# Kernel optimization log

Measured on AMD Instinct MI355X. Metric: run time of the kernel, lower is better.

The kernel has to match this reference:

```python
import jax, jax.numpy as jnp
import numpy as np
from jax import lax

BOX_STRIDES = (32, 64, 128, 256)
MASK_STRIDE = 4
MASK_SIZE = 28
PATCH = 512
TOPK = 64
SCORE_TH = 0.5
IOU_TH = 0.5
MASK_TH = 0.5


def setup_inputs():
    key = jax.random.key(0)
    ks = jax.random.split(key, 10)
    d = {}
    d["pred0"] = jax.random.normal(ks[0], (2, 6, 16, 16), jnp.float32)
    d["pred1"] = jax.random.normal(ks[1], (2, 6, 8, 8), jnp.float32)
    d["pred2"] = jax.random.normal(ks[2], (2, 6, 4, 4), jnp.float32)
    d["pred3"] = jax.random.normal(ks[3], (2, 6, 2, 2), jnp.float32)
    d["feat0"] = jax.random.normal(ks[4], (2, 64, 128, 128), jnp.float32)
    d["feat1"] = jax.random.normal(ks[5], (2, 64, 64, 64), jnp.float32)
    d["feat2"] = jax.random.normal(ks[6], (2, 64, 32, 32), jnp.float32)
    d["feat3"] = jax.random.normal(ks[7], (2, 64, 16, 16), jnp.float32)
    d["w1"] = jax.random.normal(ks[8], (128, 256, 3, 3), jnp.float32) * 0.05
    d["b1"] = jnp.zeros((128,), jnp.float32)
    d["w2"] = jax.random.normal(ks[9], (1, 128, 1, 1), jnp.float32) * 0.05
    d["b2"] = jnp.zeros((1,), jnp.float32)
    return d


def _decode_level(pred, stride):
    # pred: [B, 6, H, W] -> [B, H*W, 6], (cx,cy)=(p+grid)*stride, wh=exp(p)*stride
    B, no, H, W = pred.shape
    p = pred.transpose(0, 2, 3, 1).reshape(B, H * W, no)
    gy, gx = jnp.meshgrid(jnp.arange(H), jnp.arange(W), indexing="ij")
    grid = jnp.stack([gx.ravel(), gy.ravel()], axis=-1).astype(p.dtype)  # [HW,2] (x,y)
    xy = (p[..., 0:2] + grid) * stride
    wh = jnp.exp(p[..., 2:4]) * stride
    return jnp.concatenate([xy, wh, p[..., 4:]], axis=-1)


def _iou_matrix(b):
    # b: [K,4] xyxy
    area = jnp.clip(b[:, 2] - b[:, 0], 0) * jnp.clip(b[:, 3] - b[:, 1], 0)
    ix0 = jnp.maximum(b[:, None, 0], b[None, :, 0])
    iy0 = jnp.maximum(b[:, None, 1], b[None, :, 1])
    ix1 = jnp.minimum(b[:, None, 2], b[None, :, 2])
    iy1 = jnp.minimum(b[:, None, 3], b[None, :, 3])
    inter = jnp.clip(ix1 - ix0, 0) * jnp.clip(iy1 - iy0, 0)
    union = area[:, None] + area[None, :] - inter
    return inter / jnp.maximum(union, 1e-9)


def _nms_keep(boxes, labels, valid):
    # boxes already sorted by descending score; batched NMS via per-class coord offset
    off = labels.astype(boxes.dtype)[:, None] * (PATCH * 8.0)
    iou = _iou_matrix(boxes + off)
    idx = jnp.arange(TOPK)

    def body(i, keep):
        sup = keep[i] & (iou[i] > IOU_TH) & (idx > i)
        return keep & ~sup

    return lax.fori_loop(0, TOPK, body, valid)


def _roi_align_one(feat, box):
    # feat: [C,Hf,Wf]; box: [4] xyxy in image coords (spatial_scale=1/MASK_STRIDE)
    # torchvision-style aligned=False, one bilinear sample per bin center
    C, Hf, Wf = feat.shape
    b = box / MASK_STRIDE
    bw = (b[2] - b[0]) / MASK_SIZE
    bh = (b[3] - b[1]) / MASK_SIZE
    xs = b[0] + (jnp.arange(MASK_SIZE, dtype=feat.dtype) + 0.5) * bw
    ys = b[1] + (jnp.arange(MASK_SIZE, dtype=feat.dtype) + 0.5) * bh
    x = jnp.clip(jnp.broadcast_to(xs[None, :], (MASK_SIZE, MASK_SIZE)), 0.0, Wf - 1.0)
    y = jnp.clip(jnp.broadcast_to(ys[:, None], (MASK_SIZE, MASK_SIZE)), 0.0, Hf - 1.0)
    x0 = jnp.floor(x).astype(jnp.int32)
    y0 = jnp.floor(y).astype(jnp.int32)
    x1 = jnp.minimum(x0 + 1, Wf - 1)
    y1 = jnp.minimum(y0 + 1, Hf - 1)
    fx = x - x0
    fy = y - y0
    v00 = feat[:, y0, x0]
    v01 = feat[:, y0, x1]
    v10 = feat[:, y1, x0]
    v11 = feat[:, y1, x1]
    return (v00 * (1 - fy) * (1 - fx) + v01 * (1 - fy) * fx
            + v10 * fy * (1 - fx) + v11 * fy * fx)  # [C,S,S]


def _paste_one(mask_soft, box_int):
    # nearest-neighbor upsample of [S,S] mask into its box on a [P,P] canvas
    x0, y0, x1, y1 = box_int[0], box_int[1], box_int[2], box_int[3]
    h = y1 - y0 + 1
    w = x1 - x0 + 1
    ys = jnp.arange(PATCH, dtype=jnp.int32)
    xs = jnp.arange(PATCH, dtype=jnp.int32)
    iy = jnp.clip((ys - y0) * MASK_SIZE // h, 0, MASK_SIZE - 1)
    ix = jnp.clip((xs - x0) * MASK_SIZE // w, 0, MASK_SIZE - 1)
    g = mask_soft[iy][:, ix]  # [P,P]
    inside = ((ys >= y0) & (ys <= y1))[:, None] & ((xs >= x0) & (xs <= x1))[None, :]
    return jnp.where(inside, g, 0.0)


def _conv(x, w, b, pad):
    y = lax.conv_general_dilated(x, w, (1, 1), pad, dimension_numbers=("NCHW", "OIHW", "NCHW"))
    return y + b[None, :, None, None]


def _pipeline(pred0, pred1, pred2, pred3, feat0, feat1, feat2, feat3, w1, b1, w2, b2):
    # box branch: decode per-level predictions
    yolo = jnp.concatenate(
        [_decode_level(p, s) for p, s in zip([pred0, pred1, pred2, pred3], BOX_STRIDES)],
        axis=1,
    )  # [B,N,6]
    B = yolo.shape[0]
    cx, cy, w_, h_ = yolo[..., 0], yolo[..., 1], yolo[..., 2], yolo[..., 3]
    boxes = jnp.stack([cx - w_ / 2, cy - h_ / 2, cx + w_ / 2, cy + h_ / 2], axis=-1)
    scores = jax.nn.sigmoid(yolo[..., 4])
    labels = jnp.argmax(yolo[..., 5:], axis=-1)
    valid = scores > SCORE_TH
    top_scores, top_idx = lax.top_k(jnp.where(valid, scores, 0.0), TOPK)
    boxes_k = jnp.take_along_axis(boxes, top_idx[..., None], axis=1)  # [B,K,4]
    labels_k = jnp.take_along_axis(labels, top_idx, axis=1)
    valid_k = top_scores > SCORE_TH
    keep = jax.vmap(_nms_keep)(boxes_k, labels_k, valid_k)  # [B,K] bool

    # mask branch: merge mask feats at the first level's resolution (nearest)
    H0, W0 = feat0.shape[2], feat0.shape[3]
    merged = jnp.concatenate(
        [feat0] + [jax.image.resize(f, (B, f.shape[1], H0, W0), "nearest") for f in [feat1, feat2, feat3]],
        axis=1,
    )  # [B,256,H0,W0]
    rois = jax.vmap(lambda f, bx: jax.vmap(lambda bb: _roi_align_one(f, bb))(bx))(merged, boxes_k)
    C = rois.shape[2]
    x = rois.reshape(B * TOPK, C, MASK_SIZE, MASK_SIZE)
    hdn = jax.nn.silu(_conv(x, w1, b1, "SAME"))
    logits = _conv(hdn, w2, b2, "SAME")  # [B*K,1,S,S]
    soft = jax.nn.sigmoid(logits).reshape(B, TOPK, MASK_SIZE, MASK_SIZE)

    box_int = jnp.clip(boxes_k, 0, PATCH - 1).astype(jnp.int32)
    pasted = jax.vmap(jax.vmap(_paste_one))(soft, box_int)  # [B,K,P,P]
    return top_scores, boxes_k, labels_k, pasted, keep


def reference(pred0, pred1, pred2, pred3, feat0, feat1, feat2, feat3, w1, b1, w2, b2):
    top_scores, boxes_k, labels_k, pasted, keep = _pipeline(
        pred0, pred1, pred2, pred3, feat0, feat1, feat2, feat3, w1, b1, w2, b2
    )
    out_scores = top_scores * keep
    bin_masks = (pasted > MASK_TH) & keep[:, :, None, None]
    return out_scores, boxes_k, labels_k.astype(jnp.int32), bin_masks, keep
```

## Files before the change

### kernel.cpp

```cpp
#include <hip/hip_runtime.h>
#include <hip/hip_bf16.h>
#include <cstdint>

#define NTOPK 64
#define A_TOT 340
#define MS 28

#define OFF_SCORES 0
#define OFF_BOXES  128
#define OFF_LABELS 640
#define OFF_MASKS  768
#define OFF_KEEP   33555200ull

typedef __attribute__((ext_vector_type(4))) float f32x4;
typedef long fp8x8;

__device__ __forceinline__ float sigmoidf_(float x) { return 1.f / (1.f + expf(-x)); }
__device__ __forceinline__ float bf2f(unsigned u) {
  return __uint_as_float(u << 16);
}
__device__ __forceinline__ unsigned short f2bf(float f) {
  __hip_bfloat16 h = __float2bfloat16(f);
  return *(unsigned short*)&h;
}

__global__ __launch_bounds__(256) void k_prep(
    const float* __restrict__ p0, const float* __restrict__ p1,
    const float* __restrict__ p2, const float* __restrict__ p3,
    const float* __restrict__ f0, const float* __restrict__ f1,
    const float* __restrict__ f2, const float* __restrict__ f3,
    const float* __restrict__ w1,
    float* __restrict__ out,
    float* __restrict__ ws_boxes, int* __restrict__ ws_keep,
    int* __restrict__ ws_boxint,
    unsigned char* __restrict__ wt, unsigned short* __restrict__ mg)
{
  __shared__ __align__(16) char smem_raw[128 * 260 * 2];
  const int bid = blockIdx.x;
  const int t = threadIdx.x;

  if (bid < 2) {
    const int b = bid;
    float* sc = (float*)smem_raw;
    float(*bx)[4] = (float(*)[4])(sc + A_TOT);
    float* tk_score = (float*)(bx + A_TOT);
    float(*tk_box)[4] = (float(*)[4])(tk_score + 64);

    for (int a = t; a < A_TOT; a += 256) {
      const float* pp; int W, HW, la; float stride;
      if (a < 256)      { pp = p0; W = 16; HW = 256; la = a;       stride = 32.f;  }
      else if (a < 320) { pp = p1; W = 8;  HW = 64;  la = a - 256; stride = 64.f;  }
      else if (a < 336) { pp = p2; W = 4;  HW = 16;  la = a - 320; stride = 128.f; }
      else              { pp = p3; W = 2;  HW = 4;   la = a - 336; stride = 256.f; }
      const float* base = pp + (size_t)b * 6 * HW + la;
      float v0 = base[0], v1 = base[HW], v2 = base[2 * HW], v3 = base[3 * HW], v4 = base[4 * HW];
      int gx = la % W, gy = la / W;
      float cx = (v0 + (float)gx) * stride;
      float cy = (v1 + (float)gy) * stride;
      float w_ = expf(v2) * stride;
      float h_ = expf(v3) * stride;
      float score = sigmoidf_(v4);
      sc[a] = (score > 0.5f) ? score : 0.f;
      bx[a][0] = cx - 0.5f * w_;
      bx[a][1] = cy - 0.5f * h_;
      bx[a][2] = cx + 0.5f * w_;
      bx[a][3] = cy + 0.5f * h_;
    }
    __syncthreads();

    for (int a = t; a < A_TOT; a += 256) {
      float my = sc[a];
      int rank = 0;
      for (int j = 0; j < A_TOT; ++j) {
        float o = sc[j];
        rank += (o > my) || (o == my && j < a);
      }
      if (rank < NTOPK) {
        tk_score[rank] = my;
        tk_box[rank][0] = bx[a][0];
        tk_box[rank][1] = bx[a][1];
        tk_box[rank][2] = bx[a][2];
        tk_box[rank][3] = bx[a][3];
      }
    }
    __syncthreads();

    if (t < NTOPK) {
      float x0 = tk_box[t][0], y0 = tk_box[t][1];
      float x1 = tk_box[t][2], y1 = tk_box[t][3];
      float s = tk_score[t];
      float area = fmaxf(x1 - x0, 0.f) * fmaxf(y1 - y0, 0.f);
      int keep = (s > 0.5f) ? 1 : 0;
      for (int i = 0; i < NTOPK - 1; ++i) {
        int   ki = __shfl(keep, i);
        float a0 = __shfl(x0, i);
        float c0 = __shfl(y0, i);
        float a1 = __shfl(x1, i);
        float c1 = __shfl(y1, i);
        float ai = __shfl(area, i);
        if (ki && t > i && keep) {
          float ix0 = fmaxf(a0, x0), iy0 = fmaxf(c0, y0);
          float ix1 = fminf(a1, x1), iy1 = fminf(c1, y1);
          float inter = fmaxf(ix1 - ix0, 0.f) * fmaxf(iy1 - iy0, 0.f);
          float uni = ai + area - inter;
          float iou = inter / fmaxf(uni, 1e-9f);
          if (iou > 0.5f) keep = 0;
        }
      }
      int box = b * NTOPK + t;
      out[OFF_SCORES + box] = keep ? s : 0.f;
      float bv[4] = {x0, y0, x1, y1};
      #pragma unroll
      for (int c = 0; c < 4; ++c) {
        out[OFF_BOXES + box * 4 + c] = bv[c];
        ws_boxes[box * 4 + c] = bv[c];
        float bc = fminf(fmaxf(bv[c], 0.f), 511.f);
        ws_boxint[box * 4 + c] = (int)bc;
      }
      out[OFF_LABELS + box] = 0.f;
      out[OFF_KEEP + box] = keep ? 1.f : 0.f;
      ws_keep[box] = keep;
    }
    return;
  }

  if (bid < 130) {
    const int co = bid - 2;
    const int ci = t;
    const int c = ci >> 5, cil = ci & 31;
    const int cq = co >> 5, col = co & 31;
    const int slot = ((cil >> 3) ^ ((col >> 2) & 3)) * 8 + (cil & 7);
    const float* src = w1 + ((size_t)co * 256 + ci) * 9;
    #pragma unroll
    for (int tap = 0; tap < 9; ++tap) {
      unsigned u = __builtin_amdgcn_cvt_pk_fp8_f32(src[tap], 0.f, 0, false);
      wt[(((size_t)(cq * 8 + c) * 9 + tap)) * 1024 + col * 32 + slot] =
          (unsigned char)(u & 0xff);
    }
    return;
  }

  {
    const int idx = bid - 130;
    const int b = idx >> 7;
    const int y = idx & 127;
    unsigned short* tile = (unsigned short*)smem_raw;
    const int x = t & 127, ch = t >> 7;

    {
      const float* src = f0 + ((size_t)b * 64) * 16384 + y * 128 + x;
      for (int cc = 0; cc < 32; ++cc) {
        int cl = ch * 32 + cc;
        tile[x * 260 + cl] = f2bf(src[(size_t)cl * 16384]);
      }
    }
    {
      const float* src = f1 + ((size_t)b * 64) * 4096 + (y >> 1) * 64 + (x >> 1);
      for (int cc = 0; cc < 32; ++cc) {
        int cl = ch * 32 + cc;
        tile[x * 260 + 64 + cl] = f2bf(src[(size_t)cl * 4096]);
      }
    }
    {
      const float* src = f2 + ((size_t)b * 64) * 1024 + (y >> 2) * 32 + (x >> 2);
      for (int cc = 0; cc < 32; ++cc) {
        int cl = ch * 32 + cc;
        tile[x * 260 + 128 + cl] = f2bf(src[(size_t)cl * 1024]);
      }
    }
    {
      const float* src = f3 + ((size_t)b * 64) * 256 + (y >> 3) * 16 + (x >> 3);
      for (int cc = 0; cc < 32; ++cc) {
        int cl = ch * 32 + cc;
        tile[x * 260 + 192 + cl] = f2bf(src[(size_t)cl * 256]);
      }
    }
    __syncthreads();
    unsigned short* dst = mg + (((size_t)b * 128 + y) * 128) * 256;
    for (int it = 0; it < 32; ++it) {
      int qq = t + it * 256;
      int xx = qq >> 6, cg = qq & 63;
      *(ushort4*)(dst + xx * 256 + cg * 4) = *(ushort4*)&tile[xx * 260 + cg * 4];
    }
  }
}

__global__ __launch_bounds__(256) void k_roistage(
    const unsigned short* __restrict__ mg,
    const float* __restrict__ ws_boxes, const int* __restrict__ ws_keep,
    unsigned char* __restrict__ roi)
{
  const int boxLo = blockIdx.x & 7;
  const int r2 = blockIdx.x >> 3;
  const int r = r2 % 30;
  const int box = ((r2 / 30) << 3) | boxLo;
  if (!ws_keep[box]) return;
  const int t = threadIdx.x;
  unsigned char* rbox = roi + (size_t)box * 8 * 30 * 1024;
  const int gr = r - 1;

  if (gr < 0 || gr > 27) {
    uint2 z = {0u, 0u};
    for (int e = t; e < 1024; e += 256) {
      int chunk = e >> 7, rem = e & 127;
      int cell = rem >> 2, quad = rem & 3;
      size_t off = ((size_t)(chunk * 30 + r)) * 1024 + cell * 32 +
                   (quad ^ ((cell >> 2) & 3)) * 8;
      *(uint2*)(rbox + off) = z;
    }
    return;
  }

  __shared__ int   xa_s[MS], xb_s[MS];
  __shared__ float fx_s[MS];
  __shared__ float by_s[4];
  if (t < 4) by_s[t] = ws_boxes[box * 4 + t];
  __syncthreads();
  const float b0 = by_s[0] * 0.25f, b1_ = by_s[1] * 0.25f;
  const float b2_ = by_s[2] * 0.25f, b3_ = by_s[3] * 0.25f;
  if (t < MS) {
    float bw = (b2_ - b0) * (1.f / MS);
    float x = b0 + ((float)t + 0.5f) * bw;
    x = fminf(fmaxf(x, 0.f), 127.f);
    int x0 = (int)floorf(x);
    xa_s[t] = x0; xb_s[t] = min(x0 + 1, 127); fx_s[t] = x - (float)x0;
  }
  float bh = (b3_ - b1_) * (1.f / MS);
  float yy = b1_ + ((float)gr + 0.5f) * bh;
  yy = fminf(fmaxf(yy, 0.f), 127.f);
  int ya = (int)floorf(yy);
  int yb = min(ya + 1, 127);
  float fy = yy - (float)ya;
  __syncthreads();

  const int b = box >> 6;
  const unsigned short* mgb = mg + ((size_t)b * 128 * 128) * 256;

  for (int e = t; e < 1024; e += 256) {
    int chunk = e >> 7, rem = e & 127;
    int cell = rem >> 2, quad = rem & 3;
    size_t off = ((size_t)(chunk * 30 + r)) * 1024 + cell * 32 +
                 (quad ^ ((cell >> 2) & 3)) * 8;
    int gc = cell - 1;
    if (gc < 0 || gc > 27) {
      uint2 z = {0u, 0u};
      *(uint2*)(rbox + off) = z;
      continue;
    }
    int U = chunk * 4 + quad;
    int xa = xa_s[gc], xb = xb_s[gc];
    float fx = fx_s[gc];
    float w00 = (1.f - fy) * (1.f - fx), w01 = (1.f - fy) * fx;
    float w10 = fy * (1.f - fx),         w11 = fy * fx;
    uint4 A = *(const uint4*)(mgb + ((size_t)(ya * 128 + xa)) * 256 + U * 8);
    uint4 B = *(const uint4*)(mgb + ((size_t)(ya * 128 + xb)) * 256 + U * 8);
    uint4 C = *(const uint4*)(mgb + ((size_t)(yb * 128 + xa)) * 256 + U * 8);
    uint4 D = *(const uint4*)(mgb + ((size_t)(yb * 128 + xb)) * 256 + U * 8);
    const unsigned* pa = (const unsigned*)&A;
    const unsigned* pb = (const unsigned*)&B;
    const unsigned* pc = (const unsigned*)&C;
    const unsigned* pd = (const unsigned*)&D;
    float f[8];
    #pragma unroll
    for (int k2 = 0; k2 < 4; ++k2) {
      f[2 * k2] = bf2f(pa[k2] & 0xffffu) * w00 + bf2f(pb[k2] & 0xffffu) * w01 +
                  bf2f(pc[k2] & 0xffffu) * w10 + bf2f(pd[k2] & 0xffffu) * w11;
      f[2 * k2 + 1] = bf2f(pa[k2] >> 16) * w00 + bf2f(pb[k2] >> 16) * w01 +
                      bf2f(pc[k2] >> 16) * w10 + bf2f(pd[k2] >> 16) * w11;
    }
    unsigned o0 = __builtin_amdgcn_cvt_pk_fp8_f32(f[0], f[1], 0, false);
    o0 = __builtin_amdgcn_cvt_pk_fp8_f32(f[2], f[3], o0, true);
    unsigned o1 = __builtin_amdgcn_cvt_pk_fp8_f32(f[4], f[5], 0, false);
    o1 = __builtin_amdgcn_cvt_pk_fp8_f32(f[6], f[7], o1, true);
    uint2 pk; pk.x = o0; pk.y = o1;
    *(uint2*)(rbox + off) = pk;
  }
}

__global__ __launch_bounds__(256, 4) void k_conv(
    const unsigned char* __restrict__ roi,
    const unsigned char* __restrict__ wt,
    const float* __restrict__ b1, const float* __restrict__ w2,
    const int* __restrict__ ws_keep,
    float* __restrict__ ws_logit4)
{
  const int bid = blockIdx.x;
  const int boxLo = bid & 7;
  const int r1 = bid >> 3;
  const int cq = r1 & 3;
  const int q = (r1 >> 2) & 3;
  const int box = ((r1 >> 4) << 3) | boxLo;
  if (!ws_keep[box]) return;
  const int t = threadIdx.x;
  const int lane = t & 63, wv = t >> 6;
  const int laneN = lane & 15, kg = lane >> 4;

  __shared__ __align__(16) unsigned char lds[18432];

  int badd[4][3];
  bool act[4];
  #pragma unroll
  for (int i = 0; i < 4; ++i) {
    int tile = wv * 4 + i;
    act[i] = (tile * 16) < 196;
    int p = tile * 16 + laneN;
    if (p > 195) p = 195;
    int py = p / 28, px = p - py * 28;
    #pragma unroll
    for (int dx = 0; dx < 3; ++dx) {
      int cell = px + dx;
      badd[i][dx] = 9216 + py * 1024 + cell * 32 + (kg ^ ((cell >> 2) & 3)) * 8;
    }
  }
  const int aswz = (kg ^ ((laneN >> 2) & 3)) * 8;

  f32x4 acc[2][4];
  #pragma unroll
  for (int m = 0; m < 2; ++m)
    #pragma unroll
    for (int i = 0; i < 4; ++i) acc[m][i] = (f32x4){0.f, 0.f, 0.f, 0.f};

  const uint4* rbase = (const uint4*)roi;
  const uint4* wbase = (const uint4*)wt;

  uint4 ga0, ga1, ga2;
  uint4 gb0, gb1, gb2;
  auto issue_load = [&](int c) {
    const uint4* wa = wbase + (size_t)(cq * 8 + c) * 576;
    ga0 = wa[t]; ga1 = wa[t + 256];
    if (t < 64) ga2 = wa[t + 512];
    const uint4* s = rbase + ((size_t)(box * 8 + c) * 30 + q * 7) * 64;
    gb0 = s[t]; gb1 = s[t + 256];
    if (t < 64) gb2 = s[t + 512];
  };

  issue_load(0);
  #pragma unroll 1
  for (int c = 0; c < 8; ++c) {
    {
      uint4* da = (uint4*)lds;
      da[t] = ga0; da[t + 256] = ga1;
      if (t < 64) da[t + 512] = ga2;
      uint4* db = (uint4*)(lds + 9216);
      db[t] = gb0; db[t + 256] = gb1;
      if (t < 64) db[t + 512] = gb2;
    }
    __syncthreads();
    if (c < 7) issue_load(c + 1);
    #pragma unroll
    for (int tap = 0; tap < 9; ++tap) {
      const int dy = tap / 3, dx = tap % 3;
      fp8x8 av0 = *(const fp8x8*)(lds + tap * 1024 + laneN * 32 + aswz);
      fp8x8 av1 = *(const fp8x8*)(lds + tap * 1024 + 512 + laneN * 32 + aswz);
      #pragma unroll
      for (int i = 0; i < 4; ++i) {
        if (act[i]) {
          fp8x8 bv = *(const fp8x8*)(lds + badd[i][dx] + dy * 1024);
          acc[0][i] = __builtin_amdgcn_mfma_f32_16x16x32_fp8_fp8(av0, bv, acc[0][i], 0, 0, 0);
          acc[1][i] = __builtin_amdgcn_mfma_f32_16x16x32_fp8_fp8(av1, bv, acc[1][i], 0, 0, 0);
        }
      }
    }
    __syncthreads();
  }

  float b1v[2][4], w2v[2][4];
  #pragma unroll
  for (int m = 0; m < 2; ++m)
    #pragma unroll
    for (int r = 0; r < 4; ++r) {
      int co = cq * 32 + m * 16 + kg * 4 + r;
      b1v[m][r] = b1[co];
      w2v[m][r] = w2[co];
    }
  #pragma unroll
  for (int i = 0; i < 4; ++i) {
    if (!act[i]) continue;
    float part = 0.f;
    #pragma unroll
    for (int m = 0; m < 2; ++m)
      #pragma unroll
      for (int r = 0; r < 4; ++r) {
        float h = acc[m][i][r] + b1v[m][r];
        part = fmaf(w2v[m][r], h * sigmoidf_(h), part);
      }
    part += __shfl_xor(part, 16);
    part += __shfl_xor(part, 32);
    int p = (wv * 4 + i) * 16 + laneN;
    if (kg == 0 && p < 196)
      ws_logit4[((size_t)box * 4 + cq) * 784 + q * 196 + p] = part;
  }
}

__global__ __launch_bounds__(256) void k_paste(
    const float* __restrict__ ws_logit4, const int* __restrict__ ws_keep,
    const int* __restrict__ ws_boxint, const float* __restrict__ b2,
    float* __restrict__ out)
{
  const int box = blockIdx.x >> 4;
  const int yo  = blockIdx.x & 15;
  const int t = threadIdx.x;
  float* mb = out + OFF_MASKS + (size_t)box * 262144 + (size_t)yo * 32 * 512;

  if (!ws_keep[box]) {
    f32x4 z = {0.f, 0.f, 0.f, 0.f};
    f32x4* p = (f32x4*)mb;
    for (int e = t; e < 4096; e += 256)
      __builtin_nontemporal_store(z, p + e);
    return;
  }

  __shared__ float soft[784];
  __shared__ int iys[32];
  __shared__ int bi[4];
  if (t < 4) bi[t] = ws_boxint[box * 4 + t];
  __syncthreads();
  const int x0 = bi[0], y0 = bi[1], x1 = bi[2], y1 = bi[3];
  const int w = x1 - x0 + 1, h = y1 - y0 + 1;
  const float b2v = b2[0];
  const float* l0 = ws_logit4 + (size_t)box * 4 * 784;

  for (int e = t; e < 784; e += 256)
    soft[e] = sigmoidf_(l0[e] + l0[784 + e] + l0[1568 + e] + l0[2352 + e] + b2v);
  if (t < 32) {
    int Y = yo * 32 + t;
    int vy = (Y - y0) * MS;
    int iy = (vy >= 0) ? (vy / h) : 0;
    iys[t] = min(max(iy, 0), MS - 1);
  }
  __syncthreads();

  const int c4 = (t & 127) * 4;
  const int rr = t >> 7;
  int ixr[4];
  bool inx[4];
  #pragma unroll
  for (int u = 0; u < 4; ++u) {
    int X = c4 + u;
    int vx = (X - x0) * MS;
    int ix = (vx >= 0) ? (vx / w) : 0;
    ixr[u] = min(max(ix, 0), MS - 1);
    inx[u] = (X >= x0) && (X <= x1);
  }

  int prev_iy = -1;
  f32x4 v = {0.f, 0.f, 0.f, 0.f};
  #pragma unroll 1
  for (int it = 0; it < 16; ++it) {
    int Yl = it * 2 + rr;
    int Y = yo * 32 + Yl;
    f32x4 o;
    if (Y >= y0 && Y <= y1) {
      int iy = iys[Yl];
      if (iy != prev_iy) {
        prev_iy = iy;
        #pragma unroll
        for (int u = 0; u < 4; ++u)
          v[u] = (inx[u] && soft[iy * MS + ixr[u]] > 0.5f) ? 1.f : 0.f;
      }
      o = v;
    } else {
      o = (f32x4){0.f, 0.f, 0.f, 0.f};
    }
    __builtin_nontemporal_store(o, (f32x4*)(mb + (size_t)Yl * 512 + c4));
  }
}

extern "C" void kernel_launch(void* const* d_in, const int* in_sizes, int n_in,
                              void* d_out, int out_size, void* d_ws, size_t ws_size,
                              hipStream_t stream) {
  const float* p0 = (const float*)d_in[0];
  const float* p1 = (const float*)d_in[1];
  const float* p2 = (const float*)d_in[2];
  const float* p3 = (const float*)d_in[3];
  const float* f0 = (const float*)d_in[4];
  const float* f1 = (const float*)d_in[5];
  const float* f2 = (const float*)d_in[6];
  const float* f3 = (const float*)d_in[7];
  const float* w1 = (const float*)d_in[8];
  const float* b1 = (const float*)d_in[9];
  const float* w2 = (const float*)d_in[10];
  const float* b2 = (const float*)d_in[11];
  float* out = (float*)d_out;

  float* wsf = (float*)d_ws;
  float*          ws_boxes  = wsf;
  int*            ws_keep   = (int*)(wsf + 512);
  int*            ws_boxint = (int*)(wsf + 640);
  float*          ws_logit4 = wsf + 1152;
  unsigned char*  ws_wt     = (unsigned char*)(wsf + 402560);
  unsigned short* ws_merged = (unsigned short*)(wsf + 476288);
  unsigned char*  ws_roi    = (unsigned char*)(wsf + 4670592);

  k_prep<<<386, 256, 0, stream>>>(p0, p1, p2, p3, f0, f1, f2, f3, w1,
                                  out, ws_boxes, ws_keep, ws_boxint,
                                  ws_wt, ws_merged);
  k_roistage<<<3840, 256, 0, stream>>>(ws_merged, ws_boxes, ws_keep, ws_roi);
  k_conv<<<2048, 256, 0, stream>>>(ws_roi, ws_wt, b1, w2, ws_keep, ws_logit4);
  k_paste<<<2048, 256, 0, stream>>>(ws_logit4, ws_keep, ws_boxint, b2, out);
}
```

Before: 263.8 us.

## Double-buffer ROI tiles in LDS, read weights from global, rotate tile assignment

The conv kernel now double-buffers the ROI input tile in LDS, so only one barrier per channel chunk is needed instead of two, and it stops staging weights in LDS, reading the fp8 weight fragments directly from global/cache memory instead. Tile-to-wave assignment is interleaved (tile = rot + 4*i) with a per-block rotation, which balances the inactive tail tiles across waves. This aims to cut barrier stalls and LDS store traffic. The cost is per-tap global-memory latency on the A-operand loads.

```diff
diff --git a/kernel.cpp b/kernel.cpp
--- a/kernel.cpp
+++ b/kernel.cpp
@@ -295,13 +295,15 @@
   const int lane = t & 63, wv = t >> 6;
   const int laneN = lane & 15, kg = lane >> 4;
 
-  __shared__ __align__(16) unsigned char lds[18432];
+  const int rot = (wv + (bid >> 3)) & 3;
+
+  __shared__ __align__(16) unsigned char lds[2][9216];
 
   int badd[4][3];
   bool act[4];
   #pragma unroll
   for (int i = 0; i < 4; ++i) {
-    int tile = wv * 4 + i;
+    int tile = rot + 4 * i;
     act[i] = (tile * 16) < 196;
     int p = tile * 16 + laneN;
     if (p > 195) p = 195;
@@ -309,7 +311,7 @@
     #pragma unroll
     for (int dx = 0; dx < 3; ++dx) {
       int cell = px + dx;
-      badd[i][dx] = 9216 + py * 1024 + cell * 32 + (kg ^ ((cell >> 2) & 3)) * 8;
+      badd[i][dx] = py * 1024 + cell * 32 + (kg ^ ((cell >> 2) & 3)) * 8;
     }
   }
   const int aswz = (kg ^ ((laneN >> 2) & 3)) * 8;
@@ -321,47 +323,49 @@
     for (int i = 0; i < 4; ++i) acc[m][i] = (f32x4){0.f, 0.f, 0.f, 0.f};
 
   const uint4* rbase = (const uint4*)roi;
-  const uint4* wbase = (const uint4*)wt;
-
-  uint4 ga0, ga1, ga2;
+  const unsigned char* wbase = wt + (size_t)cq * 8 * 9216;
+
   uint4 gb0, gb1, gb2;
   auto issue_load = [&](int c) {
-    const uint4* wa = wbase + (size_t)(cq * 8 + c) * 576;
-    ga0 = wa[t]; ga1 = wa[t + 256];
-    if (t < 64) ga2 = wa[t + 512];
     const uint4* s = rbase + ((size_t)(box * 8 + c) * 30 + q * 7) * 64;
     gb0 = s[t]; gb1 = s[t + 256];
     if (t < 64) gb2 = s[t + 512];
   };
+  auto write_lds = [&](int buf) {
+    uint4* db = (uint4*)lds[buf];
+    db[t] = gb0; db[t + 256] = gb1;
+    if (t < 64) db[t + 512] = gb2;
+  };
 
   issue_load(0);
+  write_lds(0);
+  __syncthreads();
+
+  int cur = 0;
   #pragma unroll 1
   for (int c = 0; c < 8; ++c) {
-    {
-      uint4* da = (uint4*)lds;
-      da[t] = ga0; da[t + 256] = ga1;
-      if (t < 64) da[t + 512] = ga2;
-      uint4* db = (uint4*)(lds + 9216);
-      db[t] = gb0; db[t + 256] = gb1;
-      if (t < 64) db[t + 512] = gb2;
-    }
-    __syncthreads();
     if (c < 7) issue_load(c + 1);
+    const unsigned char* wa = wbase + (size_t)c * 9216;
+    const unsigned char* bb = lds[cur];
     #pragma unroll
     for (int tap = 0; tap < 9; ++tap) {
       const int dy = tap / 3, dx = tap % 3;
-      fp8x8 av0 = *(const fp8x8*)(lds + tap * 1024 + laneN * 32 + aswz);
-      fp8x8 av1 = *(const fp8x8*)(lds + tap * 1024 + 512 + laneN * 32 + aswz);
+      fp8x8 av0 = *(const fp8x8*)(wa + tap * 1024 + laneN * 32 + aswz);
+      fp8x8 av1 = *(const fp8x8*)(wa + tap * 1024 + 512 + laneN * 32 + aswz);
       #pragma unroll
       for (int i = 0; i < 4; ++i) {
         if (act[i]) {
-          fp8x8 bv = *(const fp8x8*)(lds + badd[i][dx] + dy * 1024);
+          fp8x8 bv = *(const fp8x8*)(bb + badd[i][dx] + dy * 1024);
           acc[0][i] = __builtin_amdgcn_mfma_f32_16x16x32_fp8_fp8(av0, bv, acc[0][i], 0, 0, 0);
           acc[1][i] = __builtin_amdgcn_mfma_f32_16x16x32_fp8_fp8(av1, bv, acc[1][i], 0, 0, 0);
         }
       }
     }
-    __syncthreads();
+    if (c < 7) {
+      write_lds(cur ^ 1);
+      __syncthreads();
+      cur ^= 1;
+    }
   }
 
   float b1v[2][4], w2v[2][4];
@@ -386,7 +390,7 @@
       }
     part += __shfl_xor(part, 16);
     part += __shfl_xor(part, 32);
-    int p = (wv * 4 + i) * 16 + laneN;
+    int p = (rot + 4 * i) * 16 + laneN;
     if (kg == 0 && p < 196)
       ws_logit4[((size_t)box * 4 + cq) * 784 + q * 196 + p] = part;
   }
```

After: 271.4 us. 1.03x slower.

## Merge output-channel quarters into one conv block to share ROI tile loads

Applied to the files above, without the earlier changes.

The weight tensor layout is reordered so all four output-channel quarters for an input chunk are contiguous. The conv kernel now runs 512-thread blocks where each pair of waves owns one channel quarter, so one ROI tile load in LDS is shared by all 128 output channels instead of being reloaded by four separate blocks. This cuts redundant ROI global traffic and block count. In exchange it uses more LDS (about 45 KB), more accumulator registers per wave (7 tiles), and fewer, larger blocks, which may lower occupancy.

```diff
diff --git a/kernel.cpp b/kernel.cpp
--- a/kernel.cpp
+++ b/kernel.cpp
@@ -134,7 +134,7 @@
     #pragma unroll
     for (int tap = 0; tap < 9; ++tap) {
       unsigned u = __builtin_amdgcn_cvt_pk_fp8_f32(src[tap], 0.f, 0, false);
-      wt[(((size_t)(cq * 8 + c) * 9 + tap)) * 1024 + col * 32 + slot] =
+      wt[(((size_t)(c * 4 + cq) * 9 + tap)) * 1024 + col * 32 + slot] =
           (unsigned char)(u & 0xff);
     }
     return;
@@ -277,7 +277,7 @@
   }
 }
 
-__global__ __launch_bounds__(256, 4) void k_conv(
+__global__ __launch_bounds__(512, 4) void k_conv(
     const unsigned char* __restrict__ roi,
     const unsigned char* __restrict__ wt,
     const float* __restrict__ b1, const float* __restrict__ w2,
@@ -287,73 +287,76 @@
   const int bid = blockIdx.x;
   const int boxLo = bid & 7;
   const int r1 = bid >> 3;
-  const int cq = r1 & 3;
-  const int q = (r1 >> 2) & 3;
-  const int box = ((r1 >> 4) << 3) | boxLo;
+  const int q = r1 & 3;
+  const int box = ((r1 >> 2) << 3) | boxLo;
   if (!ws_keep[box]) return;
   const int t = threadIdx.x;
   const int lane = t & 63, wv = t >> 6;
+  const int cq = wv >> 1, half = wv & 1;
   const int laneN = lane & 15, kg = lane >> 4;
 
-  __shared__ __align__(16) unsigned char lds[18432];
-
-  int badd[4][3];
-  bool act[4];
+  __shared__ __align__(16) unsigned char lds[46080];
+
+  int badd[7][3];
+  bool act[7];
   #pragma unroll
-  for (int i = 0; i < 4; ++i) {
-    int tile = wv * 4 + i;
-    act[i] = (tile * 16) < 196;
+  for (int i = 0; i < 7; ++i) {
+    int tile = half * 7 + i;
+    act[i] = tile < 13;
     int p = tile * 16 + laneN;
     if (p > 195) p = 195;
     int py = p / 28, px = p - py * 28;
     #pragma unroll
     for (int dx = 0; dx < 3; ++dx) {
       int cell = px + dx;
-      badd[i][dx] = 9216 + py * 1024 + cell * 32 + (kg ^ ((cell >> 2) & 3)) * 8;
+      badd[i][dx] = 36864 + py * 1024 + cell * 32 + (kg ^ ((cell >> 2) & 3)) * 8;
     }
   }
   const int aswz = (kg ^ ((laneN >> 2) & 3)) * 8;
 
-  f32x4 acc[2][4];
+  f32x4 acc[2][7];
   #pragma unroll
   for (int m = 0; m < 2; ++m)
     #pragma unroll
-    for (int i = 0; i < 4; ++i) acc[m][i] = (f32x4){0.f, 0.f, 0.f, 0.f};
+    for (int i = 0; i < 7; ++i) acc[m][i] = (f32x4){0.f, 0.f, 0.f, 0.f};
 
   const uint4* rbase = (const uint4*)roi;
   const uint4* wbase = (const uint4*)wt;
 
-  uint4 ga0, ga1, ga2;
-  uint4 gb0, gb1, gb2;
+  uint4 ga0, ga1, ga2, ga3, ga4;
+  uint4 gb0, gb1;
   auto issue_load = [&](int c) {
-    const uint4* wa = wbase + (size_t)(cq * 8 + c) * 576;
-    ga0 = wa[t]; ga1 = wa[t + 256];
-    if (t < 64) ga2 = wa[t + 512];
+    const uint4* wa = wbase + (size_t)c * 2304;
+    ga0 = wa[t]; ga1 = wa[t + 512]; ga2 = wa[t + 1024]; ga3 = wa[t + 1536];
+    if (t < 256) ga4 = wa[t + 2048];
     const uint4* s = rbase + ((size_t)(box * 8 + c) * 30 + q * 7) * 64;
-    gb0 = s[t]; gb1 = s[t + 256];
-    if (t < 64) gb2 = s[t + 512];
+    gb0 = s[t];
+    if (t < 64) gb1 = s[t + 512];
   };
+  auto write_lds = [&]() {
+    uint4* da = (uint4*)lds;
+    da[t] = ga0; da[t + 512] = ga1; da[t + 1024] = ga2; da[t + 1536] = ga3;
+    if (t < 256) da[t + 2048] = ga4;
+    uint4* db = (uint4*)(lds + 36864);
+    db[t] = gb0;
+    if (t < 64) db[t + 512] = gb1;
+  };
 
   issue_load(0);
+  const unsigned char* la = lds + (size_t)cq * 9216;
+
   #pragma unroll 1
   for (int c = 0; c < 8; ++c) {
-    {
-      uint4* da = (uint4*)lds;
-      da[t] = ga0; da[t + 256] = ga1;
-      if (t < 64) da[t + 512] = ga2;
-      uint4* db = (uint4*)(lds + 9216);
-      db[t] = gb0; db[t + 256] = gb1;
-      if (t < 64) db[t + 512] = gb2;
-    }
+    write_lds();
     __syncthreads();
     if (c < 7) issue_load(c + 1);
     #pragma unroll
     for (int tap = 0; tap < 9; ++tap) {
-      const int dy = tap / 3, dx = tap % 3;
-      fp8x8 av0 = *(const fp8x8*)(lds + tap * 1024 + laneN * 32 + aswz);
-      fp8x8 av1 = *(const fp8x8*)(lds + tap * 1024 + 512 + laneN * 32 + aswz);
+      const int dy = tap / 3, dx = tap - dy * 3;
+      fp8x8 av0 = *(const fp8x8*)(la + tap * 1024 + laneN * 32 + aswz);
+      fp8x8 av1 = *(const fp8x8*)(la + tap * 1024 + 512 + laneN * 32 + aswz);
       #pragma unroll
-      for (int i = 0; i < 4; ++i) {
+      for (int i = 0; i < 7; ++i) {
         if (act[i]) {
           fp8x8 bv = *(const fp8x8*)(lds + badd[i][dx] + dy * 1024);
           acc[0][i] = __builtin_amdgcn_mfma_f32_16x16x32_fp8_fp8(av0, bv, acc[0][i], 0, 0, 0);
@@ -374,7 +377,7 @@
       w2v[m][r] = w2[co];
     }
   #pragma unroll
-  for (int i = 0; i < 4; ++i) {
+  for (int i = 0; i < 7; ++i) {
     if (!act[i]) continue;
     float part = 0.f;
     #pragma unroll
@@ -386,7 +389,7 @@
       }
     part += __shfl_xor(part, 16);
     part += __shfl_xor(part, 32);
-    int p = (wv * 4 + i) * 16 + laneN;
+    int p = (half * 7 + i) * 16 + laneN;
     if (kg == 0 && p < 196)
       ws_logit4[((size_t)box * 4 + cq) * 784 + q * 196 + p] = part;
   }
@@ -496,6 +499,6 @@
                                   out, ws_boxes, ws_keep, ws_boxint,
                                   ws_wt, ws_merged);
   k_roistage<<<3840, 256, 0, stream>>>(ws_merged, ws_boxes, ws_keep, ws_roi);
-  k_conv<<<2048, 256, 0, stream>>>(ws_roi, ws_wt, b1, w2, ws_keep, ws_logit4);
+  k_conv<<<512, 512, 0, stream>>>(ws_roi, ws_wt, b1, w2, ws_keep, ws_logit4);
   k_paste<<<2048, 256, 0, stream>>>(ws_logit4, ws_keep, ws_boxint, b2, out);
 }
```

After: 263.2 us. No clear change (-0.2%).
